# Kernel tuning notes

Measured on AMD Instinct MI355X. Metric: run time of the kernel, lower is better.

The kernel has to match this reference:

```python
import jax, jax.numpy as jnp
import numpy as np

EPS = 1e-8  # F.cosine_similarity eps
K = 2       # prompt_length


def setup_inputs() -> dict:
    key = jax.random.key(0)
    k1, k2, k3, k4 = jax.random.split(key, 4)
    B, DIM, NP, D = 32, 64, 4, 1024   # P: [batch, dim, N_p, D]; D == V (rows of stored table)
    E, VC = 768, 32000                 # stored table [V=D, E]; f_e: E -> vocab_dim=VC
    P = jax.random.normal(k1, (B, DIM, NP, D), dtype=jnp.float32)
    we_stored = jax.random.normal(k2, (D, E), dtype=jnp.float32) * 0.02
    fe_w = jax.random.normal(k3, (VC, E), dtype=jnp.float32) * 0.02
    fe_b = jax.random.normal(k4, (VC,), dtype=jnp.float32) * 0.02
    return {"P": P, "we_stored": we_stored, "fe_w": fe_w, "fe_b": fe_b}


def reference(P, we_stored, fe_w, fe_b):
    # word_embeddings = f_e(stored).t()  ->  [vocab_dim, V] == [VC, D]
    T = (we_stored @ fe_w.T + fe_b).T            # [VC, D]
    B, DIM, NP, D = P.shape
    # Cosine sim of each tiled embedding row (repeated N_p times) vs flattened P_i:
    #   dot(tiled_w, P_flat) = w . sum_j P[..., j, :]
    #   ||tiled_w|| = sqrt(N_p) * ||w||
    s = P.sum(axis=2)                                             # [B, DIM, D]
    w_norm = jnp.maximum(jnp.sqrt(jnp.float32(NP)) * jnp.linalg.norm(T, axis=1), EPS)   # [VC]
    p_norm = jnp.maximum(jnp.linalg.norm(P.reshape(B, DIM, -1), axis=-1), EPS)          # [B, DIM]
    scores = jnp.einsum('bdk,vk->bdv', s, T) / (w_norm[None, None, :] * p_norm[..., None])  # [B, DIM, VC]
    values, indices = jax.lax.top_k(scores, K)                    # [B, DIM, K]
    e_k = T[indices]                                              # [B, DIM, K, D]
    Z = jnp.concatenate([e_k, P], axis=2)                         # [B, DIM, NP+K, D]
    return Z, values
```

## Files before the change

### kernel.cpp

```cpp
#include <hip/hip_runtime.h>
#include <hip/hip_bf16.h>
#include <math.h>

#define B_    32
#define DIM_  64
#define NP_   4
#define D_    1024
#define E_    768
#define VC_   32000
#define R_    2048
#define KTOP  2
#define EPS_  1e-8f
#define NCB   250
#define NCAND 8

#define T_OFF    ((size_t)0)
#define S_OFF    (T_OFF + (size_t)VC_ * D_)
#define INVW_OFF (S_OFF + (size_t)R_ * D_)
#define INVP_OFF (INVW_OFF + VC_)
#define WSQ_OFF  (INVP_OFF + R_)
#define PV_OFF   (WSQ_OFF + VC_)
#define PI_OFF   (PV_OFF + (size_t)R_ * NCB * 2)
#define SB_OFF   (PI_OFF + (size_t)R_ * NCB * 2)
#define TB_OFF   (SB_OFF + (size_t)R_ * D_ / 2)
#define WH_OFF   (TB_OFF + (size_t)VC_ * D_ / 2)
#define WL_OFF   (WH_OFF + (size_t)D_ * E_ / 2)
#define CAND_OFF (WL_OFF + (size_t)D_ * E_ / 2)
#define TIDX_OFF (CAND_OFF + (size_t)R_ * NCAND)
#define AH_OFF   (TIDX_OFF + (size_t)R_ * 2)
#define AL_OFF   (AH_OFF + (size_t)VC_ * E_ / 2)

#define NEG_INF (-3.4e38f)

typedef __bf16 bf16x8 __attribute__((ext_vector_type(8)));
typedef unsigned short u16x8 __attribute__((ext_vector_type(8)));
typedef float  f32x4  __attribute__((ext_vector_type(4)));

__device__ __forceinline__ void async_ld16(const void* gptr, void* lptr) {
    __builtin_amdgcn_global_load_lds(
        (const __attribute__((address_space(1))) void*)(uintptr_t)gptr,
        (__attribute__((address_space(3))) void*)(unsigned)(uintptr_t)lptr,
        16, 0, 0);
}

__device__ __forceinline__ bool better(float v, int i, float bv, int bi) {
    return (v > bv) || (v == bv && i < bi);
}

__global__ __launch_bounds__(256) void k_zero(float* __restrict__ wsq) {
    int i = blockIdx.x * 256 + threadIdx.x;
    if (i < VC_) wsq[i] = 0.f;
}

__global__ __launch_bounds__(256) void k_split(const float* __restrict__ x,
                                               unsigned short* __restrict__ hi,
                                               unsigned short* __restrict__ lo) {
    int i = (blockIdx.x * 256 + threadIdx.x) * 4;
    float4 v = *(const float4*)(x + i);
    ushort4 h, l;
    __bf16 b;
    b = (__bf16)v.x; h.x = __builtin_bit_cast(unsigned short, b); l.x = __builtin_bit_cast(unsigned short, (__bf16)(v.x - (float)b));
    b = (__bf16)v.y; h.y = __builtin_bit_cast(unsigned short, b); l.y = __builtin_bit_cast(unsigned short, (__bf16)(v.y - (float)b));
    b = (__bf16)v.z; h.z = __builtin_bit_cast(unsigned short, b); l.z = __builtin_bit_cast(unsigned short, (__bf16)(v.z - (float)b));
    b = (__bf16)v.w; h.w = __builtin_bit_cast(unsigned short, b); l.w = __builtin_bit_cast(unsigned short, (__bf16)(v.w - (float)b));
    *(ushort4*)(hi + i) = h;
    *(ushort4*)(lo + i) = l;
}

__global__ __launch_bounds__(256) void k_sum_pnorm(const float* __restrict__ P,
                                                   float* __restrict__ s,
                                                   unsigned short* __restrict__ sb,
                                                   float* __restrict__ invp) {
    int r = blockIdx.x;
    int t = threadIdx.x;
    const float* base = P + (size_t)r * NP_ * D_;
    float4 acc = make_float4(0.f, 0.f, 0.f, 0.f);
    float sq = 0.f;
#pragma unroll
    for (int np = 0; np < NP_; ++np) {
        float4 v = *(const float4*)(base + (size_t)np * D_ + t * 4);
        acc.x += v.x; acc.y += v.y; acc.z += v.z; acc.w += v.w;
        sq += v.x * v.x + v.y * v.y + v.z * v.z + v.w * v.w;
    }
    *(float4*)(s + (size_t)r * D_ + t * 4) = acc;
    ushort4 o;
    __bf16 b;
    b = (__bf16)acc.x; o.x = __builtin_bit_cast(unsigned short, b);
    b = (__bf16)acc.y; o.y = __builtin_bit_cast(unsigned short, b);
    b = (__bf16)acc.z; o.z = __builtin_bit_cast(unsigned short, b);
    b = (__bf16)acc.w; o.w = __builtin_bit_cast(unsigned short, b);
    *(ushort4*)(sb + (size_t)r * D_ + t * 4) = o;

    __shared__ float red[256];
    red[t] = sq;
    __syncthreads();
    for (int off = 128; off > 0; off >>= 1) {
        if (t < off) red[t] += red[t + off];
        __syncthreads();
    }
    if (t == 0) invp[r] = 1.0f / fmaxf(sqrtf(red[0]), EPS_);
}

__global__ __launch_bounds__(512) void k_gemm_T_mfma(const unsigned short* __restrict__ Ahg,
                                                     const unsigned short* __restrict__ Alg,
                                                     const unsigned short* __restrict__ Bhg,
                                                     const unsigned short* __restrict__ Blg,
                                                     const float* __restrict__ bias,
                                                     float* __restrict__ T,
                                                     unsigned short* __restrict__ Tb,
                                                     float* __restrict__ wsq) {
    __shared__ __align__(16) unsigned short Ash[3][256 * 32];
    __shared__ __align__(16) unsigned short Asl[3][256 * 32];
    __shared__ __align__(16) unsigned short Bsh[3][128 * 32];
    __shared__ __align__(16) unsigned short Bsl[3][128 * 32];

    int tid = threadIdx.x;
    int wid = tid >> 6, lane = tid & 63;
    int quad = lane >> 4, l15 = lane & 15;
    int wm = wid >> 1, wn = wid & 1;
    int id  = blockIdx.x;
    int swz = (id & 7) * 125 + (id >> 3);
    int v0 = (swz >> 3) * 256;
    int d0 = (swz & 7) * 128;

    f32x4 acc[4][4];
#pragma unroll
    for (int i = 0; i < 4; ++i)
#pragma unroll
        for (int j = 0; j < 4; ++j) acc[i][j] = f32x4{0.f, 0.f, 0.f, 0.f};

    int r_lane = lane >> 2;
    int slot   = lane & 3;

#define STAGE_T(buf, kk)                                                           \
    {                                                                              \
_Pragma("unroll")                                                                  \
        for (int j = 0; j < 2; ++j) {                                              \
            int rowt = j * 128 + wid * 16 + r_lane;                                \
            int ss = (slot - (rowt >> 1)) & 3;                                     \
            async_ld16(Ahg + (size_t)(v0 + rowt) * E_ + (kk) + ss * 8,             \
                       (void*)(Ash[buf] + (j * 128 + wid * 16) * 32));             \
            async_ld16(Alg + (size_t)(v0 + rowt) * E_ + (kk) + ss * 8,             \
                       (void*)(Asl[buf] + (j * 128 + wid * 16) * 32));             \
        }                                                                          \
        {                                                                          \
            int rowb = wid * 16 + r_lane;                                          \
            int ssb = (slot - (rowb >> 1)) & 3;                                    \
            async_ld16(Bhg + (size_t)(d0 + rowb) * E_ + (kk) + ssb * 8,            \
                       (void*)(Bsh[buf] + (wid * 16) * 32));                       \
            async_ld16(Blg + (size_t)(d0 + rowb) * E_ + (kk) + ssb * 8,            \
                       (void*)(Bsl[buf] + (wid * 16) * 32));                       \
        }                                                                          \
    }

    STAGE_T(0, 0);
    STAGE_T(1, 32);

    const int NT = E_ / 32;
    int cur = 0;
    for (int kt = 0; kt < NT; ++kt) {
        int kn = (kt + 2 < NT) ? (kt + 2) * 32 : kt * 32;
        int nb = cur + 2; if (nb >= 3) nb -= 3;
        STAGE_T(nb, kn);

        asm volatile("s_waitcnt vmcnt(12)" ::: "memory");
        __builtin_amdgcn_s_barrier();
        asm volatile("" ::: "memory");

        bf16x8 fbh[4], fbl[4];
#pragma unroll
        for (int nt = 0; nt < 4; ++nt) {
            int row = wn * 64 + nt * 16 + l15;
            int ps = (quad + (row >> 1)) & 3;
            int off = row * 32 + ps * 8;
            fbh[nt] = *(const bf16x8*)(Bsh[cur] + off);
            fbl[nt] = *(const bf16x8*)(Bsl[cur] + off);
        }
        __builtin_amdgcn_s_setprio(1);
#pragma unroll
        for (int mt = 0; mt < 4; ++mt) {
            int row = wm * 64 + mt * 16 + l15;
            int ps = (quad + (row >> 1)) & 3;
            int off = row * 32 + ps * 8;
            bf16x8 fah = *(const bf16x8*)(Ash[cur] + off);
            bf16x8 fal = *(const bf16x8*)(Asl[cur] + off);
#pragma unroll
            for (int nt = 0; nt < 4; ++nt) {
                acc[mt][nt] = __builtin_amdgcn_mfma_f32_16x16x32_bf16(fah, fbh[nt], acc[mt][nt], 0, 0, 0);
                acc[mt][nt] = __builtin_amdgcn_mfma_f32_16x16x32_bf16(fal, fbh[nt], acc[mt][nt], 0, 0, 0);
                acc[mt][nt] = __builtin_amdgcn_mfma_f32_16x16x32_bf16(fah, fbl[nt], acc[mt][nt], 0, 0, 0);
            }
        }
        __builtin_amdgcn_s_setprio(0);

        __builtin_amdgcn_sched_barrier(0);
        __builtin_amdgcn_s_barrier();
        asm volatile("" ::: "memory");
        cur = (cur == 2) ? 0 : cur + 1;
    }
#undef STAGE_T

    float sq[4][4] = {};
#pragma unroll
    for (int mt = 0; mt < 4; ++mt) {
        int vbase = v0 + wm * 64 + mt * 16 + quad * 4;
        float bv[4];
#pragma unroll
        for (int rg = 0; rg < 4; ++rg) bv[rg] = bias[vbase + rg];
#pragma unroll
        for (int nt = 0; nt < 4; ++nt) {
            int d = d0 + wn * 64 + nt * 16 + l15;
#pragma unroll
            for (int rg = 0; rg < 4; ++rg) {
                float val = acc[mt][nt][rg] + bv[rg];
                T[(size_t)(vbase + rg) * D_ + d] = val;
                __bf16 vb = (__bf16)val;
                Tb[(size_t)(vbase + rg) * D_ + d] = __builtin_bit_cast(unsigned short, vb);
                sq[mt][rg] += val * val;
            }
        }
    }
#pragma unroll
    for (int mt = 0; mt < 4; ++mt)
#pragma unroll
        for (int rg = 0; rg < 4; ++rg) {
            float p = sq[mt][rg];
            p += __shfl_xor(p, 1); p += __shfl_xor(p, 2);
            p += __shfl_xor(p, 4); p += __shfl_xor(p, 8);
            if (l15 == 0) atomicAdd(&wsq[v0 + wm * 64 + mt * 16 + quad * 4 + rg], p);
        }
}

__global__ __launch_bounds__(256) void k_invw(const float* __restrict__ wsq,
                                              float* __restrict__ invw) {
    int v = blockIdx.x * 256 + threadIdx.x;
    if (v < VC_) invw[v] = 1.0f / fmaxf(2.0f * sqrtf(wsq[v]), EPS_);
}

__global__ __launch_bounds__(512) void k_scores_mfma(const unsigned short* __restrict__ Tb,
                                                     const unsigned short* __restrict__ sb,
                                                     const float* __restrict__ invw,
                                                     float* __restrict__ pval,
                                                     int* __restrict__ pidx) {
    __shared__ __align__(16) unsigned short As[4][256 * 32];
    __shared__ __align__(16) unsigned short Bs[4][256 * 32];

    int tid = threadIdx.x;
    int wid = tid >> 6, lane = tid & 63;
    int quad = lane >> 4, l15 = lane & 15;
    int wm = wid >> 2, wn = wid & 3;
    int id   = blockIdx.x;
    int swz  = (id & 7) * 125 + (id >> 3);
    int vblk = swz >> 3;
    int rblk = swz & 7;
    int v0 = vblk * 256;
    int r0 = rblk * 256;

    f32x4 acc[8][4];
#pragma unroll
    for (int i = 0; i < 8; ++i)
#pragma unroll
        for (int j = 0; j < 4; ++j) acc[i][j] = f32x4{0.f, 0.f, 0.f, 0.f};

    int r_lane = lane >> 2;
    int slot   = lane & 3;

#define STAGE_SC(buf, kk)                                                          \
    {                                                                              \
_Pragma("unroll")                                                                  \
        for (int j = 0; j < 2; ++j) {                                              \
            int rowt = j * 128 + wid * 16 + r_lane;                                \
            int ss = (slot - (rowt >> 1)) & 3;                                     \
            async_ld16(Tb + (size_t)(v0 + rowt) * D_ + (kk) + ss * 8,              \
                       (void*)(As[buf] + (j * 128 + wid * 16) * 32));              \
            async_ld16(sb + (size_t)(r0 + rowt) * D_ + (kk) + ss * 8,              \
                       (void*)(Bs[buf] + (j * 128 + wid * 16) * 32));              \
        }                                                                          \
    }

    STAGE_SC(0, 0);
    STAGE_SC(1, 32);
    STAGE_SC(2, 64);

    const int NT = D_ / 32;
    for (int kt = 0; kt < NT; ++kt) {
        int cur = kt & 3;
        int kn  = (kt + 3 < NT) ? (kt + 3) * 32 : kt * 32;
        STAGE_SC((kt + 3) & 3, kn);

        asm volatile("s_waitcnt vmcnt(12)" ::: "memory");
        __builtin_amdgcn_s_barrier();
        asm volatile("" ::: "memory");

        bf16x8 bfr[4];
#pragma unroll
        for (int nt = 0; nt < 4; ++nt) {
            int row = wn * 64 + nt * 16 + l15;
            int ps = (quad + (row >> 1)) & 3;
            bfr[nt] = *(const bf16x8*)(Bs[cur] + row * 32 + ps * 8);
        }
        __builtin_amdgcn_s_setprio(1);
#pragma unroll
        for (int mt = 0; mt < 8; ++mt) {
            int row = wm * 128 + mt * 16 + l15;
            int ps = (quad + (row >> 1)) & 3;
            bf16x8 af = *(const bf16x8*)(As[cur] + row * 32 + ps * 8);
#pragma unroll
            for (int nt = 0; nt < 4; ++nt)
                acc[mt][nt] = __builtin_amdgcn_mfma_f32_16x16x32_bf16(af, bfr[nt], acc[mt][nt], 0, 0, 0);
        }
        __builtin_amdgcn_s_setprio(0);

        __builtin_amdgcn_sched_barrier(0);
        __builtin_amdgcn_s_barrier();
        asm volatile("" ::: "memory");
    }
#undef STAGE_SC

    float iw[8][4];
#pragma unroll
    for (int mt = 0; mt < 8; ++mt)
#pragma unroll
        for (int rg = 0; rg < 4; ++rg)
            iw[mt][rg] = invw[v0 + wm * 128 + mt * 16 + quad * 4 + rg];

#pragma unroll
    for (int nt = 0; nt < 4; ++nt) {
        float b1 = NEG_INF, b2 = NEG_INF;
        int i1 = 0x7fffffff, i2 = 0x7fffffff;
#pragma unroll
        for (int mt = 0; mt < 8; ++mt)
#pragma unroll
            for (int rg = 0; rg < 4; ++rg) {
                float val = acc[mt][nt][rg] * iw[mt][rg];
                int v = v0 + wm * 128 + mt * 16 + quad * 4 + rg;
                if (better(val, v, b1, i1)) { b2 = b1; i2 = i1; b1 = val; i1 = v; }
                else if (better(val, v, b2, i2)) { b2 = val; i2 = v; }
            }
#pragma unroll
        for (int off = 16; off <= 32; off <<= 1) {
            float o1 = __shfl_xor(b1, off), o2 = __shfl_xor(b2, off);
            int  oi1 = __shfl_xor(i1, off), oi2 = __shfl_xor(i2, off);
            if (better(o1, oi1, b1, i1)) {
                if (better(b1, i1, o2, oi2)) { b2 = b1; i2 = i1; } else { b2 = o2; i2 = oi2; }
                b1 = o1; i1 = oi1;
            } else if (better(o1, oi1, b2, i2)) { b2 = o1; i2 = oi1; }
        }
        if (quad == 0) {
            int rl = wn * 64 + nt * 16 + l15;
            size_t off = ((size_t)(r0 + rl) * NCB + vblk * 2 + wm) * 2;
            pval[off] = b1;     pidx[off] = i1;
            pval[off + 1] = b2; pidx[off + 1] = i2;
        }
    }
}

__global__ __launch_bounds__(256) void k_topk8(const float* __restrict__ pval,
                                               const int* __restrict__ pidx,
                                               int* __restrict__ cands) {
    int r = blockIdx.x, t = threadIdx.x;
    __shared__ float v[512];
    __shared__ int  id[512];
    for (int c = t; c < 512; c += 256) {
        if (c < NCB * 2) { v[c] = pval[(size_t)r * NCB * 2 + c]; id[c] = pidx[(size_t)r * NCB * 2 + c]; }
        else             { v[c] = NEG_INF; id[c] = 0x7fffffff; }
    }
    __syncthreads();
    if (t == 0) {
        float bv[NCAND]; int bi[NCAND];
#pragma unroll
        for (int j = 0; j < NCAND; ++j) { bv[j] = NEG_INF; bi[j] = 0x7fffffff; }
        for (int c = 0; c < NCB * 2; ++c) {
            float x = v[c]; int xi = id[c];
            if (better(x, xi, bv[NCAND - 1], bi[NCAND - 1])) {
                int j = NCAND - 1;
                while (j > 0 && better(x, xi, bv[j - 1], bi[j - 1])) {
                    bv[j] = bv[j - 1]; bi[j] = bi[j - 1]; --j;
                }
                bv[j] = x; bi[j] = xi;
            }
        }
#pragma unroll
        for (int j = 0; j < NCAND; ++j) cands[r * NCAND + j] = bi[j];
    }
}

__global__ __launch_bounds__(256) void k_rescore(const float* __restrict__ s,
                                                 const float* __restrict__ T,
                                                 const int* __restrict__ cands,
                                                 const float* __restrict__ invw,
                                                 const float* __restrict__ invp,
                                                 float* __restrict__ outv,
                                                 int* __restrict__ tidx) {
    int r = blockIdx.x, t = threadIdx.x;
    int cg = t >> 5, l32 = t & 31;
    int c = cands[r * NCAND + cg];
    const float* Trow = T + (size_t)c * D_;
    const float* srow = s + (size_t)r * D_;
    float p = 0.f;
#pragma unroll
    for (int j = 0; j < 8; ++j) {
        int e = (j * 32 + l32) * 4;
        float4 a = *(const float4*)(srow + e);
        float4 b = *(const float4*)(Trow + e);
        p += a.x * b.x + a.y * b.y + a.z * b.z + a.w * b.w;
    }
#pragma unroll
    for (int off = 16; off >= 1; off >>= 1) p += __shfl_xor(p, off);
    __shared__ float sc[NCAND];
    if (l32 == 0) sc[cg] = p;
    __syncthreads();
    if (t == 0) {
        float ip = invp[r];
        float b1 = NEG_INF, b2 = NEG_INF;
        int i1 = 0x7fffffff, i2 = 0x7fffffff;
#pragma unroll
        for (int j = 0; j < NCAND; ++j) {
            int ci = cands[r * NCAND + j];
            float val = sc[j] * invw[ci] * ip;
            if (better(val, ci, b1, i1)) { b2 = b1; i2 = i1; b1 = val; i1 = ci; }
            else if (better(val, ci, b2, i2)) { b2 = val; i2 = ci; }
        }
        outv[(size_t)r * 2 + 0] = b1;
        outv[(size_t)r * 2 + 1] = b2;
        tidx[r * 2 + 0] = i1;
        tidx[r * 2 + 1] = i2;
    }
}

__global__ __launch_bounds__(256) void k_writeZ(const float* __restrict__ P,
                                                const float* __restrict__ T,
                                                const int* __restrict__ tidx,
                                                float* __restrict__ out) {
    int blk = blockIdx.x;
    int r = blk / 6, j = blk - r * 6;
    const float* src;
    if (j < KTOP) src = T + (size_t)tidx[r * 2 + j] * D_;
    else          src = P + ((size_t)r * NP_ + (j - KTOP)) * D_;
    float4 v = *(const float4*)(src + threadIdx.x * 4);
    *(float4*)(out + ((size_t)r * 6 + j) * D_ + threadIdx.x * 4) = v;
}

extern "C" void kernel_launch(void* const* d_in, const int* in_sizes, int n_in,
                              void* d_out, int out_size, void* d_ws, size_t ws_size,
                              hipStream_t stream) {
    const float* P   = (const float*)d_in[0];
    const float* we  = (const float*)d_in[1];
    const float* few = (const float*)d_in[2];
    const float* feb = (const float*)d_in[3];
    float* out = (float*)d_out;
    float* ws  = (float*)d_ws;

    float* T    = ws + T_OFF;
    float* s    = ws + S_OFF;
    float* invw = ws + INVW_OFF;
    float* invp = ws + INVP_OFF;
    float* wsq  = ws + WSQ_OFF;
    float* pval = ws + PV_OFF;
    int*   pidx = (int*)(ws + PI_OFF);
    unsigned short* sb  = (unsigned short*)(ws + SB_OFF);
    unsigned short* Tb  = (unsigned short*)(ws + TB_OFF);
    unsigned short* weh = (unsigned short*)(ws + WH_OFF);
    unsigned short* wel = (unsigned short*)(ws + WL_OFF);
    int*   cands = (int*)(ws + CAND_OFF);
    int*   tidx  = (int*)(ws + TIDX_OFF);
    unsigned short* fewh = (unsigned short*)(ws + AH_OFF);
    unsigned short* fewl = (unsigned short*)(ws + AL_OFF);
    float* outv = out + (size_t)R_ * 6 * D_;

    k_zero<<<(VC_ + 255) / 256, 256, 0, stream>>>(wsq);
    k_split<<<(D_ * E_) / 1024, 256, 0, stream>>>(we, weh, wel);
    k_split<<<((size_t)VC_ * E_) / 1024, 256, 0, stream>>>(few, fewh, fewl);
    k_sum_pnorm<<<R_, 256, 0, stream>>>(P, s, sb, invp);
    k_gemm_T_mfma<<<1000, 512, 0, stream>>>(fewh, fewl, weh, wel, feb, T, Tb, wsq);
    k_invw<<<(VC_ + 255) / 256, 256, 0, stream>>>(wsq, invw);
    k_scores_mfma<<<1000, 512, 0, stream>>>(Tb, sb, invw, pval, pidx);
    k_topk8<<<R_, 256, 0, stream>>>(pval, pidx, cands);
    k_rescore<<<R_, 256, 0, stream>>>(s, T, cands, invw, invp, outv, tidx);
    k_writeZ<<<R_ * 6, 256, 0, stream>>>(P, T, tidx, out);
}
```

Measured before the change: 676.8 us.

## Store T as bf16 hi/lo pair, fuse zeroing and P copy into earlier kernels

Replaces the fp32 T table write (131 MB) with two bf16 halves (hi and lo), so T traffic drops from fp32+bf16 to two bf16 arrays. The rescore and Z-write kernels rebuild fp32 values from the pair. The P rows are copied into Z inside the sum/norm kernel, and the wsq zeroing moves into the we split kernel, which cuts launches and lets k_writeZ handle only the top-k rows. The hi+lo reconstruction is not bit-exact with fp32 T. Tl reuses the old T region, which is now free.

```diff
diff --git a/kernel.cpp b/kernel.cpp
--- a/kernel.cpp
+++ b/kernel.cpp
@@ -15,6 +15,7 @@
 #define NCAND 8
 
 #define T_OFF    ((size_t)0)
+#define TL_OFF   T_OFF
 #define S_OFF    (T_OFF + (size_t)VC_ * D_)
 #define INVW_OFF (S_OFF + (size_t)R_ * D_)
 #define INVP_OFF (INVW_OFF + VC_)
@@ -47,9 +48,26 @@
     return (v > bv) || (v == bv && i < bi);
 }
 
-__global__ __launch_bounds__(256) void k_zero(float* __restrict__ wsq) {
-    int i = blockIdx.x * 256 + threadIdx.x;
-    if (i < VC_) wsq[i] = 0.f;
+__device__ __forceinline__ float bfpair(unsigned short h, unsigned short l) {
+    return __uint_as_float((unsigned)h << 16) + __uint_as_float((unsigned)l << 16);
+}
+
+__global__ __launch_bounds__(256) void k_prep_we(const float* __restrict__ x,
+                                                 unsigned short* __restrict__ hi,
+                                                 unsigned short* __restrict__ lo,
+                                                 float* __restrict__ wsq) {
+    int gi = blockIdx.x * 256 + threadIdx.x;
+    if (gi < VC_) wsq[gi] = 0.f;
+    int i = gi * 4;
+    float4 v = *(const float4*)(x + i);
+    ushort4 h, l;
+    __bf16 b;
+    b = (__bf16)v.x; h.x = __builtin_bit_cast(unsigned short, b); l.x = __builtin_bit_cast(unsigned short, (__bf16)(v.x - (float)b));
+    b = (__bf16)v.y; h.y = __builtin_bit_cast(unsigned short, b); l.y = __builtin_bit_cast(unsigned short, (__bf16)(v.y - (float)b));
+    b = (__bf16)v.z; h.z = __builtin_bit_cast(unsigned short, b); l.z = __builtin_bit_cast(unsigned short, (__bf16)(v.z - (float)b));
+    b = (__bf16)v.w; h.w = __builtin_bit_cast(unsigned short, b); l.w = __builtin_bit_cast(unsigned short, (__bf16)(v.w - (float)b));
+    *(ushort4*)(hi + i) = h;
+    *(ushort4*)(lo + i) = l;
 }
 
 __global__ __launch_bounds__(256) void k_split(const float* __restrict__ x,
@@ -70,7 +88,8 @@
 __global__ __launch_bounds__(256) void k_sum_pnorm(const float* __restrict__ P,
                                                    float* __restrict__ s,
                                                    unsigned short* __restrict__ sb,
-                                                   float* __restrict__ invp) {
+                                                   float* __restrict__ invp,
+                                                   float* __restrict__ outZ) {
     int r = blockIdx.x;
     int t = threadIdx.x;
     const float* base = P + (size_t)r * NP_ * D_;
@@ -81,6 +100,7 @@
         float4 v = *(const float4*)(base + (size_t)np * D_ + t * 4);
         acc.x += v.x; acc.y += v.y; acc.z += v.z; acc.w += v.w;
         sq += v.x * v.x + v.y * v.y + v.z * v.z + v.w * v.w;
+        *(float4*)(outZ + ((size_t)r * 6 + KTOP + np) * D_ + t * 4) = v;
     }
     *(float4*)(s + (size_t)r * D_ + t * 4) = acc;
     ushort4 o;
@@ -106,8 +126,8 @@
                                                      const unsigned short* __restrict__ Bhg,
                                                      const unsigned short* __restrict__ Blg,
                                                      const float* __restrict__ bias,
-                                                     float* __restrict__ T,
-                                                     unsigned short* __restrict__ Tb,
+                                                     unsigned short* __restrict__ Th,
+                                                     unsigned short* __restrict__ Tl,
                                                      float* __restrict__ wsq) {
     __shared__ __align__(16) unsigned short Ash[3][256 * 32];
     __shared__ __align__(16) unsigned short Asl[3][256 * 32];
@@ -213,9 +233,10 @@
 #pragma unroll
             for (int rg = 0; rg < 4; ++rg) {
                 float val = acc[mt][nt][rg] + bv[rg];
-                T[(size_t)(vbase + rg) * D_ + d] = val;
-                __bf16 vb = (__bf16)val;
-                Tb[(size_t)(vbase + rg) * D_ + d] = __builtin_bit_cast(unsigned short, vb);
+                __bf16 hb = (__bf16)val;
+                __bf16 lb = (__bf16)(val - (float)hb);
+                Th[(size_t)(vbase + rg) * D_ + d] = __builtin_bit_cast(unsigned short, hb);
+                Tl[(size_t)(vbase + rg) * D_ + d] = __builtin_bit_cast(unsigned short, lb);
                 sq[mt][rg] += val * val;
             }
         }
@@ -386,7 +407,8 @@
 }
 
 __global__ __launch_bounds__(256) void k_rescore(const float* __restrict__ s,
-                                                 const float* __restrict__ T,
+                                                 const unsigned short* __restrict__ Th,
+                                                 const unsigned short* __restrict__ Tl,
                                                  const int* __restrict__ cands,
                                                  const float* __restrict__ invw,
                                                  const float* __restrict__ invp,
@@ -395,15 +417,18 @@
     int r = blockIdx.x, t = threadIdx.x;
     int cg = t >> 5, l32 = t & 31;
     int c = cands[r * NCAND + cg];
-    const float* Trow = T + (size_t)c * D_;
+    const unsigned short* hrow = Th + (size_t)c * D_;
+    const unsigned short* lrow = Tl + (size_t)c * D_;
     const float* srow = s + (size_t)r * D_;
     float p = 0.f;
 #pragma unroll
     for (int j = 0; j < 8; ++j) {
         int e = (j * 32 + l32) * 4;
         float4 a = *(const float4*)(srow + e);
-        float4 b = *(const float4*)(Trow + e);
-        p += a.x * b.x + a.y * b.y + a.z * b.z + a.w * b.w;
+        ushort4 h = *(const ushort4*)(hrow + e);
+        ushort4 l = *(const ushort4*)(lrow + e);
+        p += a.x * bfpair(h.x, l.x) + a.y * bfpair(h.y, l.y)
+           + a.z * bfpair(h.z, l.z) + a.w * bfpair(h.w, l.w);
     }
 #pragma unroll
     for (int off = 16; off >= 1; off >>= 1) p += __shfl_xor(p, off);
@@ -428,17 +453,20 @@
     }
 }
 
-__global__ __launch_bounds__(256) void k_writeZ(const float* __restrict__ P,
-                                                const float* __restrict__ T,
+__global__ __launch_bounds__(256) void k_writeZ(const unsigned short* __restrict__ Th,
+                                                const unsigned short* __restrict__ Tl,
                                                 const int* __restrict__ tidx,
                                                 float* __restrict__ out) {
     int blk = blockIdx.x;
-    int r = blk / 6, j = blk - r * 6;
-    const float* src;
-    if (j < KTOP) src = T + (size_t)tidx[r * 2 + j] * D_;
-    else          src = P + ((size_t)r * NP_ + (j - KTOP)) * D_;
-    float4 v = *(const float4*)(src + threadIdx.x * 4);
-    *(float4*)(out + ((size_t)r * 6 + j) * D_ + threadIdx.x * 4) = v;
+    int r = blk >> 1, j = blk & 1;
+    size_t c = (size_t)tidx[r * 2 + j] * D_;
+    int e = threadIdx.x * 4;
+    ushort4 h = *(const ushort4*)(Th + c + e);
+    ushort4 l = *(const ushort4*)(Tl + c + e);
+    float4 v;
+    v.x = bfpair(h.x, l.x); v.y = bfpair(h.y, l.y);
+    v.z = bfpair(h.z, l.z); v.w = bfpair(h.w, l.w);
+    *(float4*)(out + ((size_t)r * 6 + j) * D_ + e) = v;
 }
 
 extern "C" void kernel_launch(void* const* d_in, const int* in_sizes, int n_in,
@@ -451,7 +479,6 @@
     float* out = (float*)d_out;
     float* ws  = (float*)d_ws;
 
-    float* T    = ws + T_OFF;
     float* s    = ws + S_OFF;
     float* invw = ws + INVW_OFF;
     float* invp = ws + INVP_OFF;
@@ -459,7 +486,8 @@
     float* pval = ws + PV_OFF;
     int*   pidx = (int*)(ws + PI_OFF);
     unsigned short* sb  = (unsigned short*)(ws + SB_OFF);
-    unsigned short* Tb  = (unsigned short*)(ws + TB_OFF);
+    unsigned short* Th  = (unsigned short*)(ws + TB_OFF);
+    unsigned short* Tl  = (unsigned short*)(ws + TL_OFF);
     unsigned short* weh = (unsigned short*)(ws + WH_OFF);
     unsigned short* wel = (unsigned short*)(ws + WL_OFF);
     int*   cands = (int*)(ws + CAND_OFF);
@@ -468,14 +496,13 @@
     unsigned short* fewl = (unsigned short*)(ws + AL_OFF);
     float* outv = out + (size_t)R_ * 6 * D_;
 
-    k_zero<<<(VC_ + 255) / 256, 256, 0, stream>>>(wsq);
-    k_split<<<(D_ * E_) / 1024, 256, 0, stream>>>(we, weh, wel);
+    k_prep_we<<<(D_ * E_) / 1024, 256, 0, stream>>>(we, weh, wel, wsq);
     k_split<<<((size_t)VC_ * E_) / 1024, 256, 0, stream>>>(few, fewh, fewl);
-    k_sum_pnorm<<<R_, 256, 0, stream>>>(P, s, sb, invp);
-    k_gemm_T_mfma<<<1000, 512, 0, stream>>>(fewh, fewl, weh, wel, feb, T, Tb, wsq);
+    k_sum_pnorm<<<R_, 256, 0, stream>>>(P, s, sb, invp, out);
+    k_gemm_T_mfma<<<1000, 512, 0, stream>>>(fewh, fewl, weh, wel, feb, Th, Tl, wsq);
     k_invw<<<(VC_ + 255) / 256, 256, 0, stream>>>(wsq, invw);
-    k_scores_mfma<<<1000, 512, 0, stream>>>(Tb, sb, invw, pval, pidx);
+    k_scores_mfma<<<1000, 512, 0, stream>>>(Th, sb, invw, pval, pidx);
     k_topk8<<<R_, 256, 0, stream>>>(pval, pidx, cands);
-    k_rescore<<<R_, 256, 0, stream>>>(s, T, cands, invw, invp, outv, tidx);
-    k_writeZ<<<R_ * 6, 256, 0, stream>>>(P, T, tidx, out);
-}
+    k_rescore<<<R_, 256, 0, stream>>>(s, Th, Tl, cands, invw, invp, outv, tidx);
+    k_writeZ<<<R_ * 2, 256, 0, stream>>>(Th, Tl, tidx, out);
+}
```

Measured after the change: 653.4 us. -3.5%, faster.
